# Performance work log

Hardware: AMD Instinct MI355X
Metric: run time of the kernel (lower is better)

The kernel has to match this reference:

```python
import jax, jax.numpy as jnp
import numpy as np

B, N, C = 8, 2000, 512
H, W, SR = 8, 5, 2          # num_heads, window_size, sr_ratio
LN_EPS = 1e-5


def setup_inputs() -> dict:
    key = jax.random.key(0)
    ks = jax.random.split(key, 6)
    s = lambda k, shape: jax.random.normal(k, shape, jnp.float32) * 0.02
    return {
        "x": jax.random.normal(ks[0], (B, N, C), jnp.float32),
        "Wq": s(ks[1], (C, C)),      "bq": jnp.zeros((C,), jnp.float32),
        "Wkv": s(ks[2], (2 * C, C)), "bkv": jnp.zeros((2 * C,), jnp.float32),
        "Wc": s(ks[3], (C, C)),      "bc": jnp.zeros((C,), jnp.float32),
        "ln_g": jnp.ones((C,), jnp.float32), "ln_b": jnp.zeros((C,), jnp.float32),
        "Wp": s(ks[4], (C, C)),      "bp": jnp.zeros((C,), jnp.float32),
    }


def reference(x, Wq, bq, Wkv, bkv, Wc, bc, ln_g, ln_b, Wp, bp):
    Bx, Nx, Cx = x.shape
    hd = Cx // H
    scale = hd ** (-0.5)
    G = Nx // W          # number of local windows
    M = Nx // SR         # pooled length

    # q: [B,H,N,hd]
    q = (x @ Wq.T + bq).reshape(Bx, Nx, H, hd).transpose(0, 2, 1, 3)

    # local kv: [B,G,W,2,H,hd] -> k_l/v_l [B,H,G,W,hd]
    kv = (x @ Wkv.T + bkv).reshape(Bx, G, W, 2, H, hd)
    k_l = kv[:, :, :, 0].transpose(0, 3, 1, 2, 4)
    v_l = kv[:, :, :, 1].transpose(0, 3, 1, 2, 4)

    # windowed local scores: group q into windows, einsum within window
    # (equivalent to torch's repeat_interleave + per-query matmul, but no blowup)
    qw = q.reshape(Bx, H, G, W, hd)
    attn_local = jnp.einsum('bhgqd,bhgkd->bhgqk', qw, k_l).reshape(Bx, H, Nx, W) * scale

    # pooled branch: AvgPool1d(sr) -> 1x1 conv -> LayerNorm -> GELU(exact)
    xp = x.reshape(Bx, M, SR, Cx).mean(axis=2)
    xp = xp @ Wc.T + bc
    mu = xp.mean(-1, keepdims=True)
    var = xp.var(-1, keepdims=True)
    xp = (xp - mu) / jnp.sqrt(var + LN_EPS) * ln_g + ln_b
    xp = jax.nn.gelu(xp, approximate=False)

    kvp = (xp @ Wkv.T + bkv).reshape(Bx, M, 2, H, hd)
    k_p = kvp[:, :, 0].transpose(0, 2, 1, 3)   # [B,H,M,hd]
    v_p = kvp[:, :, 1].transpose(0, 2, 1, 3)

    attn_pool = jnp.einsum('bhnd,bhmd->bhnm', q, k_p) * scale  # [B,H,N,M]

    # joint softmax over local window + pooled keys
    attn = jax.nn.softmax(jnp.concatenate([attn_local, attn_pool], axis=-1), axis=-1)
    a_l = attn[..., :W].reshape(Bx, H, G, W, W)
    a_p = attn[..., W:]

    x_l = jnp.einsum('bhgqk,bhgkd->bhgqd', a_l, v_l).reshape(Bx, H, Nx, hd)
    x_p = jnp.einsum('bhnm,bhmd->bhnd', a_p, v_p)

    out = (x_l + x_p).transpose(0, 2, 1, 3).reshape(Bx, Nx, Cx)
    return out @ Wp.T + bp
```

## Files before the change

kernel.cpp:

```cpp
#include <hip/hip_runtime.h>
#include <hip/hip_bf16.h>
#include <math.h>

#define B_   8
#define N_   2000
#define C_   512
#define H_   8
#define W_   5
#define SR_  2
#define M_   1000
#define HD_  64
#define KK_  512
#define RP_  8192
#define NPAD_ 16384
#define LN_EPS_ 1e-5f
#define SCALE_  0.125f
#define QSC_    0.18033688011112042f

#define TQ_   256
#define NCH_  8
#define LT_   5
#define KSTR2 72

typedef __attribute__((ext_vector_type(8))) short bf16x8;
typedef __attribute__((ext_vector_type(4))) short short4v;
typedef __attribute__((ext_vector_type(4))) float f32x4;
typedef __attribute__((ext_vector_type(16))) float f32x16;
#define MFMA16(a,b,c) __builtin_amdgcn_mfma_f32_16x16x32_bf16(a,b,c,0,0,0)
#define MFMA32(a,b,c) __builtin_amdgcn_mfma_f32_32x32x16_bf16(a,b,c,0,0,0)

__device__ __forceinline__ short f2bf(float f) {
  unsigned u = __float_as_uint(f);
  u += 0x7FFFu + ((u >> 16) & 1u);
  return (short)(u >> 16);
}
__device__ __forceinline__ uint2 pack4bf(float4 v) {
  unsigned a = ((unsigned)(unsigned short)f2bf(v.x)) | (((unsigned)(unsigned short)f2bf(v.y)) << 16);
  unsigned b = ((unsigned)(unsigned short)f2bf(v.z)) | (((unsigned)(unsigned short)f2bf(v.w)) << 16);
  return make_uint2(a, b);
}

__device__ __forceinline__ float wave_sum(float v) {
#pragma unroll
  for (int o = 32; o > 0; o >>= 1) v += __shfl_xor(v, o);
  return v;
}

__device__ __forceinline__ void gl_lds16(const void* g, void* l) {
  __builtin_amdgcn_global_load_lds(
      (const __attribute__((address_space(1))) void*)g,
      (__attribute__((address_space(3))) void*)l, 16, 0, 0);
}

__global__ __launch_bounds__(256) void cvt_bf16(const float* __restrict__ src,
                                                short* __restrict__ dst, int n8) {
  int i = blockIdx.x * 256 + threadIdx.x;
  if (i >= n8) return;
  float4 a = reinterpret_cast<const float4*>(src)[i * 2];
  float4 b = reinterpret_cast<const float4*>(src)[i * 2 + 1];
  uint2 pa = pack4bf(a), pb = pack4bf(b);
  reinterpret_cast<uint4*>(dst)[i] = make_uint4(pa.x, pa.y, pb.x, pb.y);
}

__global__ __launch_bounds__(256) void cvt_pool(const float* __restrict__ X,
                                                short* __restrict__ Xb,
                                                short* __restrict__ Xp) {
  int idx = blockIdx.x * 256 + threadIdx.x;
  const int total = B_ * M_ * (C_ / 8);
  if (idx >= total) return;
  int row = idx / (C_ / 8);
  int c8  = idx % (C_ / 8);
  int b = row / M_, m = row % M_;
  size_t r0 = ((size_t)b * N_ + 2 * m) * C_ + c8 * 8;
  size_t r1 = r0 + C_;
  float4 a0 = *(const float4*)(X + r0), a1 = *(const float4*)(X + r0 + 4);
  float4 b0 = *(const float4*)(X + r1), b1 = *(const float4*)(X + r1 + 4);
  uint2 pa0 = pack4bf(a0), pa1 = pack4bf(a1);
  uint2 pb0 = pack4bf(b0), pb1 = pack4bf(b1);
  *(uint4*)(Xb + r0) = make_uint4(pa0.x, pa0.y, pa1.x, pa1.y);
  *(uint4*)(Xb + r1) = make_uint4(pb0.x, pb0.y, pb1.x, pb1.y);
  float4 s0, s1;
  s0.x = 0.5f * (a0.x + b0.x); s0.y = 0.5f * (a0.y + b0.y);
  s0.z = 0.5f * (a0.z + b0.z); s0.w = 0.5f * (a0.w + b0.w);
  s1.x = 0.5f * (a1.x + b1.x); s1.y = 0.5f * (a1.y + b1.y);
  s1.z = 0.5f * (a1.z + b1.z); s1.w = 0.5f * (a1.w + b1.w);
  uint2 q0 = pack4bf(s0), q1 = pack4bf(s1);
  *(uint4*)(Xp + (size_t)row * C_ + c8 * 8) = make_uint4(q0.x, q0.y, q1.x, q1.y);
}

template<int OUT_BF16>
__global__ __launch_bounds__(256) void gemm_mfma(const short* __restrict__ A,
                                                 const short* __restrict__ Bm,
                                                 const float* __restrict__ bias,
                                                 void* __restrict__ Yv,
                                                 int O, float oscale) {
  __shared__ short As[128 * 32];
  __shared__ short Bs[128 * 32];
  const int tid  = threadIdx.x;
  const int w    = tid >> 6;
  const int lane = tid & 63;
  const int g    = lane >> 4;
  const int c0   = lane & 15;
  const int wr   = w >> 1;
  const int wc   = w & 1;
  const long r0 = (long)blockIdx.y * 128;
  const long o0 = (long)blockIdx.x * 128;
  const int srow = lane >> 2;
  const int scol = (lane & 3) * 8;

  f32x4 acc[4][4];
#pragma unroll
  for (int m = 0; m < 4; ++m)
#pragma unroll
    for (int n = 0; n < 4; ++n) acc[m][n] = (f32x4){0.f, 0.f, 0.f, 0.f};

  for (int kk = 0; kk < 16; ++kk) {
    __syncthreads();
#pragma unroll
    for (int i = 0; i < 2; ++i) {
      int arow = i * 64 + w * 16;
      gl_lds16(A  + (r0 + arow + srow) * KK_ + kk * 32 + scol, &As[arow * 32]);
      gl_lds16(Bm + (o0 + arow + srow) * KK_ + kk * 32 + scol, &Bs[arow * 32]);
    }
    __syncthreads();
    bf16x8 a[4], b[4];
#pragma unroll
    for (int m = 0; m < 4; ++m) a[m] = *(const bf16x8*)&As[(wr * 64 + m * 16 + c0) * 32 + g * 8];
#pragma unroll
    for (int n = 0; n < 4; ++n) b[n] = *(const bf16x8*)&Bs[(wc * 64 + n * 16 + c0) * 32 + g * 8];
#pragma unroll
    for (int m = 0; m < 4; ++m)
#pragma unroll
      for (int n = 0; n < 4; ++n) acc[m][n] = MFMA16(a[m], b[n], acc[m][n]);
  }

#pragma unroll
  for (int m = 0; m < 4; ++m) {
    long row = r0 + wr * 64 + m * 16 + g * 4;
#pragma unroll
    for (int n = 0; n < 4; ++n) {
      long col = o0 + wc * 64 + n * 16 + c0;
      float bv = bias[col];
#pragma unroll
      for (int r = 0; r < 4; ++r) {
        float v = (acc[m][n][r] + bv) * oscale;
        if (OUT_BF16) ((short*)Yv)[(row + r) * O + col] = f2bf(v);
        else          ((float*)Yv)[(row + r) * O + col] = v;
      }
    }
  }
}

__global__ __launch_bounds__(256) void gemm_qkv(const short* __restrict__ A,
                                                const short* __restrict__ Bm,
                                                const float* __restrict__ bq,
                                                const float* __restrict__ bkv,
                                                short* __restrict__ Yq,
                                                short* __restrict__ Ykv) {
  __shared__ short As[128 * 32];
  __shared__ short Bs[128 * 32];
  const int tid  = threadIdx.x;
  const int w    = tid >> 6;
  const int lane = tid & 63;
  const int g    = lane >> 4;
  const int c0   = lane & 15;
  const int wr   = w >> 1;
  const int wc   = w & 1;
  const long r0 = (long)blockIdx.y * 128;
  const long o0 = (long)blockIdx.x * 128;
  const int srow = lane >> 2;
  const int scol = (lane & 3) * 8;

  f32x4 acc[4][4];
#pragma unroll
  for (int m = 0; m < 4; ++m)
#pragma unroll
    for (int n = 0; n < 4; ++n) acc[m][n] = (f32x4){0.f, 0.f, 0.f, 0.f};

  for (int kk = 0; kk < 16; ++kk) {
    __syncthreads();
#pragma unroll
    for (int i = 0; i < 2; ++i) {
      int arow = i * 64 + w * 16;
      gl_lds16(A  + (r0 + arow + srow) * KK_ + kk * 32 + scol, &As[arow * 32]);
      gl_lds16(Bm + (o0 + arow + srow) * KK_ + kk * 32 + scol, &Bs[arow * 32]);
    }
    __syncthreads();
    bf16x8 a[4], b[4];
#pragma unroll
    for (int m = 0; m < 4; ++m) a[m] = *(const bf16x8*)&As[(wr * 64 + m * 16 + c0) * 32 + g * 8];
#pragma unroll
    for (int n = 0; n < 4; ++n) b[n] = *(const bf16x8*)&Bs[(wc * 64 + n * 16 + c0) * 32 + g * 8];
#pragma unroll
    for (int m = 0; m < 4; ++m)
#pragma unroll
      for (int n = 0; n < 4; ++n) acc[m][n] = MFMA16(a[m], b[n], acc[m][n]);
  }

  const bool isq = (blockIdx.x < 4);
#pragma unroll
  for (int m = 0; m < 4; ++m) {
    long row = r0 + wr * 64 + m * 16 + g * 4;
#pragma unroll
    for (int n = 0; n < 4; ++n) {
      long col = o0 + wc * 64 + n * 16 + c0;
      if (isq) {
        float bv = bq[col];
#pragma unroll
        for (int r = 0; r < 4; ++r)
          Yq[(row + r) * 512 + col] = f2bf((acc[m][n][r] + bv) * QSC_);
      } else {
        long ck = col - 512;
        float bv = bkv[ck];
#pragma unroll
        for (int r = 0; r < 4; ++r)
          Ykv[(row + r) * 1024 + ck] = f2bf(acc[m][n][r] + bv);
      }
    }
  }
}

__global__ __launch_bounds__(256) void ln_gelu(const float* __restrict__ Xc,
                                               short* __restrict__ Xo,
                                               const float* __restrict__ gam,
                                               const float* __restrict__ bet) {
  const int row = blockIdx.x;
  const float* p = Xc + (size_t)row * C_;
  const int t = threadIdx.x;
  float v0 = p[t], v1 = p[t + 256];
  float s  = wave_sum(v0 + v1);
  float ss = wave_sum(v0 * v0 + v1 * v1);
  __shared__ float rs[4], rss[4];
  const int w = t >> 6, lane = t & 63;
  if (lane == 0) { rs[w] = s; rss[w] = ss; }
  __syncthreads();
  float ts  = rs[0] + rs[1] + rs[2] + rs[3];
  float tss = rss[0] + rss[1] + rss[2] + rss[3];
  float mean = ts * (1.0f / C_);
  float var  = tss * (1.0f / C_) - mean * mean;
  float rstd = rsqrtf(var + LN_EPS_);
  float u0 = (v0 - mean) * rstd * gam[t]       + bet[t];
  float u1 = (v1 - mean) * rstd * gam[t + 256] + bet[t + 256];
  Xo[(size_t)row * C_ + t]       = f2bf(u0 * 0.5f * (1.0f + erff(u0 * 0.70710678118654752f)));
  Xo[(size_t)row * C_ + t + 256] = f2bf(u1 * 0.5f * (1.0f + erff(u1 * 0.70710678118654752f)));
}

template<int MODE>
__device__ __forceinline__ void tile32(const short* Ksb, const short* Vtb,
                                       const bf16x8 qf[4],
                                       float& l_c, f32x16* o,
                                       int c, int hi, int koff)
{
  f32x16 sblk[2];
  __builtin_amdgcn_s_setprio(1);
#pragma unroll
  for (int kb = 0; kb < 2; ++kb) {
    f32x16 acc = {};
#pragma unroll
    for (int sl = 0; sl < 4; ++sl) {
      bf16x8 kf = *(const bf16x8*)&Ksb[(kb*32 + c)*KSTR2 + sl*16 + hi*8];
      acc = MFMA32(kf, qf[sl], acc);
    }
    sblk[kb] = acc;
  }
  __builtin_amdgcn_s_setprio(0);

  if (MODE == 1) {
#pragma unroll
    for (int kb = 0; kb < 2; ++kb)
#pragma unroll
      for (int r = 0; r < 16; ++r) {
        int ku = koff + kb*32 + ((r & 3) + 8*(r >> 2));
        if ((unsigned)ku >= 5u) sblk[kb][r] = -3.0e38f;
      }
  }
  if (MODE == 2) {
#pragma unroll
    for (int r = 4; r < 16; ++r) sblk[1][r] = -3.0e38f;
  }

  float rs4[4] = {0.f, 0.f, 0.f, 0.f};
  int dw[2][8];
#pragma unroll
  for (int kb = 0; kb < 2; ++kb)
#pragma unroll
    for (int i = 0; i < 8; ++i) {
      float p0 = exp2f(sblk[kb][2*i]);
      float p1 = exp2f(sblk[kb][2*i + 1]);
      rs4[i & 3] += p0 + p1;
      int d;
      asm("v_cvt_pk_bf16_f32 %0, %1, %2" : "=v"(d) : "v"(p0), "v"(p1));
      dw[kb][i] = d;
    }
  float rs = (rs4[0] + rs4[1]) + (rs4[2] + rs4[3]);
  rs += __shfl_xor(rs, 32);
  l_c += rs;

  bf16x8 pfrag[2][2];
#pragma unroll
  for (int kb = 0; kb < 2; ++kb)
#pragma unroll
    for (int kp = 0; kp < 2; ++kp) {
      union { int i[4]; bf16x8 v; } u;
      u.i[0] = dw[kb][kp*4 + 0];
      u.i[1] = dw[kb][kp*4 + 1];
      u.i[2] = dw[kb][kp*4 + 2];
      u.i[3] = dw[kb][kp*4 + 3];
      pfrag[kb][kp] = u.v;
    }

  __builtin_amdgcn_s_setprio(1);
#pragma unroll
  for (int db = 0; db < 2; ++db)
#pragma unroll
    for (int kb = 0; kb < 2; ++kb)
#pragma unroll
      for (int kp = 0; kp < 2; ++kp) {
        bf16x8 vf = *(const bf16x8*)&Vtb[(db*32 + c)*KSTR2 + kb*32 + kp*16 + hi*8];
        o[db] = MFMA32(vf, pfrag[kb][kp], o[db]);
      }
  __builtin_amdgcn_s_setprio(0);
}

__global__ __launch_bounds__(512, 4) void attn_mfma32(const short* __restrict__ Q,
                                                      const short* __restrict__ KV,
                                                      const short* __restrict__ KVP,
                                                      short* __restrict__ Oa) {
  __shared__ __align__(16) short Ks[2][64 * KSTR2];
  __shared__ __align__(16) short Vt[2][64 * KSTR2];

  const int bid   = blockIdx.x;
  const int bh    = bid & 63;
  const int chunk = bid >> 6;
  const int b     = bh >> 3;
  const int h     = bh & 7;
  const int n0    = chunk * TQ_;
  const int tid  = threadIdx.x;
  const int wq   = tid >> 6;
  const int lane = tid & 63;
  const int c    = lane & 31;
  const int hi   = lane >> 5;

  const int qabs = n0 + wq * 32 + c;
  const size_t qrow = (size_t)(b * N_ + qabs) * C_ + h * HD_;
  bf16x8 qf[4];
#pragma unroll
  for (int sl = 0; sl < 4; ++sl) qf[sl] = *(const bf16x8*)(Q + qrow + sl*16 + hi*8);

  const int qlo = (qabs / 5) * 5;
  const int klo = (n0 / 5) * 5;
  const int wlo = ((n0 + wq*32) / 5) * 5;
  const int whi = ((n0 + wq*32 + 31) / 5) * 5 + 5;

  const bool isK = (tid < 256);
  const int u    = tid & 255;
  const int kkey = u >> 3, kdq = u & 7;
  const int vkp  = u & 31, vdq = (u >> 5) & 7;
  const int svkp = (vkp & ~6) | ((vkp & 2) << 1) | ((vkp & 4) >> 1);
  bf16x8 r0v, r1v;

  auto issue = [&](const short* pb_) {
    if (isK) {
      r0v = *(const bf16x8*)(pb_ + (size_t)kkey        * (2*C_) + h*HD_ + kdq*8);
      r1v = *(const bf16x8*)(pb_ + (size_t)(kkey + 32) * (2*C_) + h*HD_ + kdq*8);
    } else {
      r0v = *(const bf16x8*)(pb_ + (size_t)(2*vkp)     * (2*C_) + C_ + h*HD_ + vdq*8);
      r1v = *(const bf16x8*)(pb_ + (size_t)(2*vkp + 1) * (2*C_) + C_ + h*HD_ + vdq*8);
    }
  };
  auto write = [&](int buf) {
    if (isK) {
      *(bf16x8*)&Ks[buf][kkey * KSTR2 + kdq * 8]        = r0v;
      *(bf16x8*)&Ks[buf][(kkey + 32) * KSTR2 + kdq * 8] = r1v;
    } else {
#pragma unroll
      for (int e = 0; e < 8; ++e) {
        unsigned wv = ((unsigned)(unsigned short)r0v[e]) | (((unsigned)(unsigned short)r1v[e]) << 16);
        *(unsigned*)&Vt[buf][(vdq*8 + e) * KSTR2 + 2*svkp] = wv;
      }
    }
  };

  const short* kvloc = KV  + (size_t)(b * N_ + klo) * (2*C_);
  const short* kvp_b = KVP + (size_t)(b * M_)       * (2*C_);

  float l_c = 0.f;
  f32x16 o[2];
  o[0] = (f32x16){}; o[1] = (f32x16){};

  issue(kvloc);
  write(0);
  __syncthreads();
  int cur = 0;

#pragma unroll 1
  for (int t = 0; t < LT_; ++t) {
    const short* nxt = (t < LT_ - 1) ? kvloc + (size_t)(t + 1) * 64 * (2*C_) : kvp_b;
    issue(nxt);
    const int base = klo + t * 64;
    if (base < whi && base + 64 > wlo)
      tile32<1>(Ks[cur], Vt[cur], qf, l_c, o, c, hi, base + 4*hi - qlo);
    write(cur ^ 1);
    __syncthreads();
    cur ^= 1;
  }
#pragma unroll 1
  for (int t = 0; t < 15; ++t) {
    issue(kvp_b + (size_t)(t + 1) * 64 * (2*C_));
    tile32<0>(Ks[cur], Vt[cur], qf, l_c, o, c, hi, 0);
    write(cur ^ 1);
    __syncthreads();
    cur ^= 1;
  }
  tile32<2>(Ks[cur], Vt[cur], qf, l_c, o, c, hi, 0);

  if (qabs < N_) {
    float inv = 1.0f / l_c;
    short* orow = Oa + ((size_t)(b * N_ + qabs)) * C_ + h * HD_;
#pragma unroll
    for (int db = 0; db < 2; ++db)
#pragma unroll
      for (int rq = 0; rq < 4; ++rq) {
        short4v sv;
#pragma unroll
        for (int i = 0; i < 4; ++i) sv[i] = f2bf(o[db][rq*4 + i] * inv);
        *(short4v*)(orow + db*32 + rq*8 + 4*hi) = sv;
      }
  }
}

extern "C" void kernel_launch(void* const* d_in, const int* in_sizes, int n_in,
                              void* d_out, int out_size, void* d_ws, size_t ws_size,
                              hipStream_t stream) {
  const float* x   = (const float*)d_in[0];
  const float* Wq  = (const float*)d_in[1];
  const float* bq  = (const float*)d_in[2];
  const float* Wkv = (const float*)d_in[3];
  const float* bkv = (const float*)d_in[4];
  const float* Wc  = (const float*)d_in[5];
  const float* bc  = (const float*)d_in[6];
  const float* lng = (const float*)d_in[7];
  const float* lnb = (const float*)d_in[8];
  const float* Wp  = (const float*)d_in[9];
  const float* bp  = (const float*)d_in[10];
  float* out = (float*)d_out;

  float* xc   = (float*)d_ws;
  short* sb   = (short*)(xc + (size_t)RP_ * 512);
  short* xb    = sb;
  short* qb    = xb   + (size_t)16000 * 512;
  short* kvb   = qb   + (size_t)NPAD_ * 512;
  short* xpb   = kvb  + (size_t)NPAD_ * 1024;
  short* xcb   = xpb  + (size_t)RP_ * 512;
  short* kvpb  = xcb  + (size_t)RP_ * 512;
  short* aoutb = kvpb + (size_t)RP_ * 1024;
  short* Wqkvb = aoutb + (size_t)16000 * 512;
  short* Wcb   = Wqkvb + (size_t)1536 * 512;
  short* Wpb   = Wcb  + (size_t)512 * 512;

  dim3 blk(256);

  cvt_pool<<<dim3((B_*M_*(C_/8) + 255)/256), blk, 0, stream>>>(x, xb, xpb);
  cvt_bf16<<<dim3((512*512/8  + 255)/256), blk, 0, stream>>>(Wq,  Wqkvb,             512*512/8);
  cvt_bf16<<<dim3((1024*512/8 + 255)/256), blk, 0, stream>>>(Wkv, Wqkvb + 512*512,   1024*512/8);
  cvt_bf16<<<dim3((512*512/8  + 255)/256), blk, 0, stream>>>(Wc,  Wcb,  512*512/8);
  cvt_bf16<<<dim3((512*512/8  + 255)/256), blk, 0, stream>>>(Wp,  Wpb,  512*512/8);

  gemm_mfma<0><<<dim3(C_/128, RP_/128), blk, 0, stream>>>(xpb, Wcb, bc, xc, C_, 1.0f);
  ln_gelu<<<dim3(B_ * M_), blk, 0, stream>>>(xc, xcb, lng, lnb);
  gemm_mfma<1><<<dim3((2*C_)/128, RP_/128), blk, 0, stream>>>(xcb, Wqkvb + 512*512, bkv, kvpb, 2*C_, 1.0f);

  gemm_qkv<<<dim3(1536/128, 16000/128), blk, 0, stream>>>(xb, Wqkvb, bq, bkv, qb, kvb);

  attn_mfma32<<<dim3(64 * NCH_), dim3(512), 0, stream>>>(qb, kvb, kvpb, aoutb);

  gemm_mfma<0><<<dim3(C_/128, 16000/128), blk, 0, stream>>>(aoutb, Wpb, bp, out, C_, 1.0f);
}
```

Before: 184.0 us.

## Stage 128-key tiles in attention and merge weight conversion launches

```diff
diff --git a/kernel.cpp b/kernel.cpp
--- a/kernel.cpp
+++ b/kernel.cpp
@@ -19,8 +19,9 @@
 
 #define TQ_   256
 #define NCH_  8
-#define LT_   5
+#define KT_   128
 #define KSTR2 72
+#define VSTR  136
 
 typedef __attribute__((ext_vector_type(8))) short bf16x8;
 typedef __attribute__((ext_vector_type(4))) short short4v;
@@ -52,14 +53,25 @@
       (__attribute__((address_space(3))) void*)l, 16, 0, 0);
 }
 
-__global__ __launch_bounds__(256) void cvt_bf16(const float* __restrict__ src,
-                                                short* __restrict__ dst, int n8) {
+__global__ __launch_bounds__(256) void cvt_all(const float* __restrict__ Wq,
+                                               const float* __restrict__ Wkv,
+                                               const float* __restrict__ Wc,
+                                               const float* __restrict__ Wp,
+                                               short* __restrict__ Wqkvb,
+                                               short* __restrict__ Wcb,
+                                               short* __restrict__ Wpb) {
   int i = blockIdx.x * 256 + threadIdx.x;
-  if (i >= n8) return;
-  float4 a = reinterpret_cast<const float4*>(src)[i * 2];
-  float4 b = reinterpret_cast<const float4*>(src)[i * 2 + 1];
+  const int nq = 512*512/8, nkv = 1024*512/8, nc = 512*512/8, np = 512*512/8;
+  if (i >= nq + nkv + nc + np) return;
+  const float* src; short* dst; int off;
+  if (i < nq)                { src = Wq;  dst = Wqkvb;             off = i; }
+  else if (i < nq + nkv)     { src = Wkv; dst = Wqkvb + 512*512;   off = i - nq; }
+  else if (i < nq + nkv + nc){ src = Wc;  dst = Wcb;               off = i - nq - nkv; }
+  else                       { src = Wp;  dst = Wpb;               off = i - nq - nkv - nc; }
+  float4 a = reinterpret_cast<const float4*>(src)[off * 2];
+  float4 b = reinterpret_cast<const float4*>(src)[off * 2 + 1];
   uint2 pa = pack4bf(a), pb = pack4bf(b);
-  reinterpret_cast<uint4*>(dst)[i] = make_uint4(pa.x, pa.y, pb.x, pb.y);
+  reinterpret_cast<uint4*>(dst)[off] = make_uint4(pa.x, pa.y, pb.x, pb.y);
 }
 
 __global__ __launch_bounds__(256) void cvt_pool(const float* __restrict__ X,
@@ -316,18 +328,18 @@
     for (int kb = 0; kb < 2; ++kb)
 #pragma unroll
       for (int kp = 0; kp < 2; ++kp) {
-        bf16x8 vf = *(const bf16x8*)&Vtb[(db*32 + c)*KSTR2 + kb*32 + kp*16 + hi*8];
+        bf16x8 vf = *(const bf16x8*)&Vtb[(db*32 + c)*VSTR + kb*32 + kp*16 + hi*8];
         o[db] = MFMA32(vf, pfrag[kb][kp], o[db]);
       }
   __builtin_amdgcn_s_setprio(0);
 }
 
-__global__ __launch_bounds__(512, 4) void attn_mfma32(const short* __restrict__ Q,
+__global__ __launch_bounds__(512, 2) void attn_mfma32(const short* __restrict__ Q,
                                                       const short* __restrict__ KV,
                                                       const short* __restrict__ KVP,
                                                       short* __restrict__ Oa) {
-  __shared__ __align__(16) short Ks[2][64 * KSTR2];
-  __shared__ __align__(16) short Vt[2][64 * KSTR2];
+  __shared__ __align__(16) short Ks[2][KT_ * KSTR2];
+  __shared__ __align__(16) short Vt[2][64 * VSTR];
 
   const int bid   = blockIdx.x;
   const int bh    = bid & 63;
@@ -357,26 +369,34 @@
   const int kkey = u >> 3, kdq = u & 7;
   const int vkp  = u & 31, vdq = (u >> 5) & 7;
   const int svkp = (vkp & ~6) | ((vkp & 2) << 1) | ((vkp & 4) >> 1);
-  bf16x8 r0v, r1v;
+  bf16x8 st0, st1, st2, st3;
 
   auto issue = [&](const short* pb_) {
     if (isK) {
-      r0v = *(const bf16x8*)(pb_ + (size_t)kkey        * (2*C_) + h*HD_ + kdq*8);
-      r1v = *(const bf16x8*)(pb_ + (size_t)(kkey + 32) * (2*C_) + h*HD_ + kdq*8);
+      st0 = *(const bf16x8*)(pb_ + (size_t)kkey        * (2*C_) + h*HD_ + kdq*8);
+      st1 = *(const bf16x8*)(pb_ + (size_t)(kkey + 32) * (2*C_) + h*HD_ + kdq*8);
+      st2 = *(const bf16x8*)(pb_ + (size_t)(kkey + 64) * (2*C_) + h*HD_ + kdq*8);
+      st3 = *(const bf16x8*)(pb_ + (size_t)(kkey + 96) * (2*C_) + h*HD_ + kdq*8);
     } else {
-      r0v = *(const bf16x8*)(pb_ + (size_t)(2*vkp)     * (2*C_) + C_ + h*HD_ + vdq*8);
-      r1v = *(const bf16x8*)(pb_ + (size_t)(2*vkp + 1) * (2*C_) + C_ + h*HD_ + vdq*8);
+      st0 = *(const bf16x8*)(pb_ + (size_t)(2*vkp)      * (2*C_) + C_ + h*HD_ + vdq*8);
+      st1 = *(const bf16x8*)(pb_ + (size_t)(2*vkp + 1)  * (2*C_) + C_ + h*HD_ + vdq*8);
+      st2 = *(const bf16x8*)(pb_ + (size_t)(2*vkp + 64) * (2*C_) + C_ + h*HD_ + vdq*8);
+      st3 = *(const bf16x8*)(pb_ + (size_t)(2*vkp + 65) * (2*C_) + C_ + h*HD_ + vdq*8);
     }
   };
   auto write = [&](int buf) {
     if (isK) {
-      *(bf16x8*)&Ks[buf][kkey * KSTR2 + kdq * 8]        = r0v;
-      *(bf16x8*)&Ks[buf][(kkey + 32) * KSTR2 + kdq * 8] = r1v;
+      *(bf16x8*)&Ks[buf][(kkey     ) * KSTR2 + kdq * 8] = st0;
+      *(bf16x8*)&Ks[buf][(kkey + 32) * KSTR2 + kdq * 8] = st1;
+      *(bf16x8*)&Ks[buf][(kkey + 64) * KSTR2 + kdq * 8] = st2;
+      *(bf16x8*)&Ks[buf][(kkey + 96) * KSTR2 + kdq * 8] = st3;
     } else {
 #pragma unroll
       for (int e = 0; e < 8; ++e) {
-        unsigned wv = ((unsigned)(unsigned short)r0v[e]) | (((unsigned)(unsigned short)r1v[e]) << 16);
-        *(unsigned*)&Vt[buf][(vdq*8 + e) * KSTR2 + 2*svkp] = wv;
+        unsigned w0 = ((unsigned)(unsigned short)st0[e]) | (((unsigned)(unsigned short)st1[e]) << 16);
+        unsigned w1 = ((unsigned)(unsigned short)st2[e]) | (((unsigned)(unsigned short)st3[e]) << 16);
+        *(unsigned*)&Vt[buf][(vdq*8 + e) * VSTR + 2*svkp]      = w0;
+        *(unsigned*)&Vt[buf][(vdq*8 + e) * VSTR + 2*svkp + 64] = w1;
       }
     }
   };
@@ -394,25 +414,33 @@
   int cur = 0;
 
 #pragma unroll 1
-  for (int t = 0; t < LT_; ++t) {
-    const short* nxt = (t < LT_ - 1) ? kvloc + (size_t)(t + 1) * 64 * (2*C_) : kvp_b;
+  for (int t = 0; t < 3; ++t) {
+    const short* nxt = (t < 2) ? kvloc + (size_t)(t + 1) * KT_ * (2*C_) : kvp_b;
     issue(nxt);
-    const int base = klo + t * 64;
-    if (base < whi && base + 64 > wlo)
-      tile32<1>(Ks[cur], Vt[cur], qf, l_c, o, c, hi, base + 4*hi - qlo);
+#pragma unroll
+    for (int s = 0; s < 2; ++s) {
+      const int base = klo + (t*2 + s) * 64;
+      if (base < whi && base + 64 > wlo)
+        tile32<1>(&Ks[cur][s*64*KSTR2], &Vt[cur][s*64], qf, l_c, o, c, hi, base + 4*hi - qlo);
+    }
     write(cur ^ 1);
     __syncthreads();
     cur ^= 1;
   }
 #pragma unroll 1
-  for (int t = 0; t < 15; ++t) {
-    issue(kvp_b + (size_t)(t + 1) * 64 * (2*C_));
-    tile32<0>(Ks[cur], Vt[cur], qf, l_c, o, c, hi, 0);
-    write(cur ^ 1);
-    __syncthreads();
-    cur ^= 1;
-  }
-  tile32<2>(Ks[cur], Vt[cur], qf, l_c, o, c, hi, 0);
+  for (int t = 0; t < 8; ++t) {
+    if (t < 7) {
+      issue(kvp_b + (size_t)(t + 1) * KT_ * (2*C_));
+      tile32<0>(&Ks[cur][0],          &Vt[cur][0],  qf, l_c, o, c, hi, 0);
+      tile32<0>(&Ks[cur][64*KSTR2],   &Vt[cur][64], qf, l_c, o, c, hi, 0);
+      write(cur ^ 1);
+      __syncthreads();
+      cur ^= 1;
+    } else {
+      tile32<0>(&Ks[cur][0],          &Vt[cur][0],  qf, l_c, o, c, hi, 0);
+      tile32<2>(&Ks[cur][64*KSTR2],   &Vt[cur][64], qf, l_c, o, c, hi, 0);
+    }
+  }
 
   if (qabs < N_) {
     float inv = 1.0f / l_c;
@@ -461,10 +489,7 @@
   dim3 blk(256);
 
   cvt_pool<<<dim3((B_*M_*(C_/8) + 255)/256), blk, 0, stream>>>(x, xb, xpb);
-  cvt_bf16<<<dim3((512*512/8  + 255)/256), blk, 0, stream>>>(Wq,  Wqkvb,             512*512/8);
-  cvt_bf16<<<dim3((1024*512/8 + 255)/256), blk, 0, stream>>>(Wkv, Wqkvb + 512*512,   1024*512/8);
-  cvt_bf16<<<dim3((512*512/8  + 255)/256), blk, 0, stream>>>(Wc,  Wcb,  512*512/8);
-  cvt_bf16<<<dim3((512*512/8  + 255)/256), blk, 0, stream>>>(Wp,  Wpb,  512*512/8);
+  cvt_all<<<dim3((2560*512/8 + 255)/256), blk, 0, stream>>>(Wq, Wkv, Wc, Wp, Wqkvb, Wcb, Wpb);
 
   gemm_mfma<0><<<dim3(C_/128, RP_/128), blk, 0, stream>>>(xpb, Wcb, bc, xc, C_, 1.0f);
   ln_gelu<<<dim3(B_ * M_), blk, 0, stream>>>(xc, xcb, lng, lnb);
```

Result: slower. 192.1 us (+4.4%).
